# Kernel tuning notes

Measured on AMD Instinct MI355X. Metric: run time of the kernel, lower is better.

## Reference

```python
import jax, jax.numpy as jnp
import numpy as np


def _ste_round(x):
    # straight-through rounding (Brevitas-style QAT)
    return x + jax.lax.stop_gradient(jnp.round(x) - x)


def _q_act_signed(x, s):
    # 4-bit signed activation fake-quant: int range [-8, 7]
    return jnp.clip(_ste_round(x / s), -8, 7) * s


def _q_relu(x, s):
    # QuantReLU: relu then 4-bit unsigned fake-quant, int range [0, 15]
    return jnp.clip(_ste_round(jax.nn.relu(x) / s), 0, 15) * s


def _q_weight(w):
    # 4-bit narrow-range per-tensor weight quant: scale = max|w|/7, range [-7, 7]
    s = jnp.max(jnp.abs(w)) / 7.0
    return jnp.clip(_ste_round(w / s), -7, 7) * s, s


def _q_bias(b, s):
    # Int32Bias: bias quantized at scale = act_scale * weight_scale (int32 range, no clamp)
    return _ste_round(b / s) * s


def _conv(x, w):
    return jax.lax.conv_general_dilated(
        x, w, (1, 1), 'VALID', dimension_numbers=('NCHW', 'OIHW', 'NCHW'))


def _maxpool_ceil(x, k=3, st=2):
    # MaxPool2d(3, 2, ceil_mode=True): pad right/bottom with -inf as needed
    def pad(n):
        out = -(-(n - k) // st) + 1
        return max(0, (out - 1) * st + k - n)
    ph, pw = pad(x.shape[2]), pad(x.shape[3])
    return jax.lax.reduce_window(
        x, -jnp.inf, jax.lax.max, (1, 1, k, k), (1, 1, st, st),
        [(0, 0), (0, 0), (0, ph), (0, pw)])


def reference(x, w1, b1, w2, b2, w3, b3, fw1, fb1, bw, bb, cw, cb,
              s_inp, s1, s2, s3, s4, s_bbox, s_conf):
    a = s_inp[0]
    x = _q_act_signed(x, a)                               # quant_inp
    # conv1 + relu1 + pool1
    wq, ws = _q_weight(w1)
    x = _conv(x, wq) + _q_bias(b1, a * ws)[None, :, None, None]
    a = s1[0]
    x = _maxpool_ceil(_q_relu(x, a))                      # [B,28,11,11]
    # conv2 + relu2 + pool2
    wq, ws = _q_weight(w2)
    x = _conv(x, wq) + _q_bias(b2, a * ws)[None, :, None, None]
    a = s2[0]
    x = _maxpool_ceil(_q_relu(x, a))                      # [B,48,4,4]
    # conv3 + relu3
    wq, ws = _q_weight(w3)
    x = _conv(x, wq) + _q_bias(b3, a * ws)[None, :, None, None]
    a = s3[0]
    x = _q_relu(x, a)                                     # [B,64,3,3]
    # QuantFlatten: transpose(3,2) then flatten -> [B, 576]
    x = jnp.transpose(x, (0, 1, 3, 2)).reshape(x.shape[0], -1)
    # fc1 + relu4
    wq, ws = _q_weight(fw1)
    x = x @ wq.T + _q_bias(fb1, a * ws)
    a = s4[0]
    x = _q_relu(x, a)                                     # [B,128]
    # heads
    wq, ws = _q_weight(bw)
    bbox = x @ wq.T + _q_bias(bb, a * ws)                 # [B,4]
    wq, ws = _q_weight(cw)
    conf = x @ wq.T + _q_bias(cb, a * ws)                 # [B,2]
    bbox = _q_act_signed(bbox, s_bbox[0])
    conf = _q_act_signed(conf, s_conf[0])
    return bbox, conf


def setup_inputs() -> dict:
    key = jax.random.key(0)
    ks = jax.random.split(key, 14)
    B = 4096
    f32 = jnp.float32
    return {
        'x': jax.random.normal(ks[0], (B, 3, 24, 24), f32),
        'w1': jax.random.normal(ks[1], (28, 3, 3, 3), f32) * 0.1,
        'b1': jax.random.normal(ks[2], (28,), f32) * 0.1,
        'w2': jax.random.normal(ks[3], (48, 28, 3, 3), f32) * 0.1,
        'b2': jax.random.normal(ks[4], (48,), f32) * 0.1,
        'w3': jax.random.normal(ks[5], (64, 48, 2, 2), f32) * 0.1,
        'b3': jax.random.normal(ks[6], (64,), f32) * 0.1,
        'fw1': jax.random.normal(ks[7], (128, 576), f32) * 0.05,
        'fb1': jax.random.normal(ks[8], (128,), f32) * 0.1,
        'bw': jax.random.normal(ks[9], (4, 128), f32) * 0.1,
        'bb': jax.random.normal(ks[10], (4,), f32) * 0.1,
        'cw': jax.random.normal(ks[11], (2, 128), f32) * 0.1,
        'cb': jax.random.normal(ks[12], (2,), f32) * 0.1,
        's_inp': jnp.ones((1,), f32),
        's1': jnp.ones((1,), f32),
        's2': jnp.ones((1,), f32),
        's3': jnp.ones((1,), f32),
        's4': jnp.ones((1,), f32),
        's_bbox': jnp.ones((1,), f32),
        's_conf': jnp.ones((1,), f32),
    }
```

## Files before the change

### kernel.cpp

```cpp
#include <hip/hip_runtime.h>
#include <hip/hip_bf16.h>
#include <math.h>

typedef __attribute__((ext_vector_type(8))) short bf16x8v;
typedef __attribute__((ext_vector_type(4))) float f32x4v;

__device__ __forceinline__ float loadT(const void* p, size_t i, int isbf) {
    if (isbf) return __bfloat162float(((const __hip_bfloat16*)p)[i]);
    return ((const float*)p)[i];
}
__device__ __forceinline__ float quantw(float v, float s) {
    return fminf(fmaxf(rintf(v / s), -7.f), 7.f) * s;
}
__device__ __forceinline__ float quantwc(float v, float s) {
    return fminf(fmaxf(rintf(v / s), -7.f), 7.f);
}
__device__ __forceinline__ float qbias(float v, float den) {
    return rintf(v / den) * den;
}
__device__ __forceinline__ float qrelu(float v, float s) {
    return fminf(fmaxf(rintf(fmaxf(v, 0.f) / s), 0.f), 15.f) * s;
}
__device__ __forceinline__ float qcode(float Cint, float bcode, float p, float snext) {
    float v = (Cint + bcode) * p;
    return fminf(fmaxf(rintf(fmaxf(v, 0.f) / snext), 0.f), 15.f);
}
__device__ __forceinline__ float bfbits(unsigned u) {
    return __uint_as_float(u << 16);
}

__global__ void k_beacon(float* out, float code) {
    if (threadIdx.x == 0 && blockIdx.x == 0) out[0] = code;
}

static constexpr int W1C  = 16;
static constexpr int B1C  = 772;
static constexpr int B2C  = 800;
static constexpr int B3C  = 848;
static constexpr int FB1C = 912;
static constexpr int BBC  = 1040;
static constexpr int CBC  = 1044;
static constexpr int FW1B = 1048;
static constexpr int W2B  = 37912;
static constexpr int W3B  = 44056;
static constexpr int BWC  = 50200;
static constexpr int CWC  = 50712;
static constexpr int PMAXF = 51000;

__device__ __constant__ int d_CHK[6]  = { 1, 4, 4, 24, 1, 1 };
__device__ __constant__ int d_POFF[7] = { 0, 1, 5, 9, 33, 34, 35 };

__global__ __launch_bounds__(256) void k_scale(
    const void* w1, const void* w2, const void* w3, const void* fw1,
    const void* bw, const void* cw,
    const void* s0p, const void* s1p, const void* s2p, const void* s3p,
    const void* s4p, const void* s5p, const void* s6p,
    float* __restrict__ ws)
{
    __shared__ float red[256];
    __shared__ float shisbf;
    const int tid = threadIdx.x, blk = blockIdx.x;
    if (tid < 64) {
        const unsigned short* hb = (const unsigned short*)w1;
        const float a = fabsf(bfbits((unsigned)hb[2 * tid]));
        const unsigned long long bz = __ballot(a == 0.f);
        const unsigned long long bs = __ballot(a > 1e-8f && a < 1e4f);
        if (tid == 0) {
            const int zeros = __popcll(bz), sane = __popcll(bs);
            shisbf = (zeros < 40 && sane >= 40) ? 1.f : 0.f;
        }
    }
    __syncthreads();
    const int isbf = shisbf > 0.5f;
    if (blk == 0) {
        if (tid == 7) ws[15] = shisbf;
        if (tid < 7) {
            const void* sp[7] = { s0p, s1p, s2p, s3p, s4p, s5p, s6p };
            const void* p = sp[tid];
            float v = *(const float*)p;
            float a = fabsf(v);
            if (!(a > 1e-6f && a < 1e6f)) {
                double d = *(const double*)p;
                double ad = fabs(d);
                if (ad > 1e-6 && ad < 1e6) v = (float)d;
                else v = bfbits((unsigned)(*(const unsigned short*)p));
            }
            ws[tid] = v;
        }
    }
    int j = 0;
    while (j < 5 && blk >= d_POFF[j + 1]) ++j;
    const int c = blk - d_POFF[j];
    const void* wp[6] = { w1, w2, w3, fw1, bw, cw };
    const int   wn[6] = { 756, 12096, 12288, 73728, 512, 256 };
    const int nw = wn[j];
    const int len = (nw + d_CHK[j] - 1) / d_CHK[j];
    const int i0 = c * len, i1 = min(i0 + len, nw);
    float m = 0.f;
    for (int i = i0 + tid; i < i1; i += 256)
        m = fmaxf(m, fabsf(loadT(wp[j], i, isbf)));
    red[tid] = m; __syncthreads();
    for (int o = 128; o > 0; o >>= 1) {
        if (tid < o) red[tid] = fmaxf(red[tid], red[tid + o]);
        __syncthreads();
    }
    if (tid == 0) ws[PMAXF + blk] = red[0];
}

__global__ __launch_bounds__(256) void k_quant(
    const void* w1, const void* b1, const void* w2, const void* b2,
    const void* w3, const void* b3, const void* fw1, const void* fb1,
    const void* bw, const void* bb, const void* cw, const void* cb,
    float* __restrict__ ws)
{
    const int tid = threadIdx.x, blk = blockIdx.x;
    const int isbf = ws[15] > 0.5f;
    auto getscale = [&](int j) {
        float m = 0.f;
        for (int t = d_POFF[j]; t < d_POFF[j + 1]; ++t)
            m = fmaxf(m, ws[PMAXF + t]);
        return m / 7.0f;
    };

    if (blk < 24) {
        const float s = getscale(3);
        const int i0 = blk * 3072, i1 = min(i0 + 3072, 73728);
        __hip_bfloat16* dst = (__hip_bfloat16*)(ws + FW1B);
        for (int i = i0 + tid; i < i1; i += 256) {
            const float q = quantwc(loadT(fw1, i, isbf), s);
            const int o = i / 576, f = i % 576;
            const int c = f / 9, fw_ = (f % 9) / 3, fh = f % 3;
            const int kk = c * 9 + fh * 3 + fw_;
            dst[(kk >> 1) * 256 + o * 2 + (kk & 1)] = __float2bfloat16(q);
        }
    } else if (blk < 28) {
        const float s = getscale(1);
        const int c = blk - 24;
        const int i0 = c * 3024, i1 = min(i0 + 3024, 12096);
        __hip_bfloat16* dst = (__hip_bfloat16*)(ws + W2B);
        for (int i = i0 + tid; i < i1; i += 256) {
            const float q = quantwc(loadT(w2, i, isbf), s);
            const int n = i / 252, k = i % 252;
            dst[n * 256 + k] = __float2bfloat16(q);
        }
        if (c == 0) {
            for (int i = tid; i < 192; i += 256) {
                const int n = i / 4, k = 252 + (i % 4);
                dst[n * 256 + k] = __float2bfloat16(0.f);
            }
        }
    } else if (blk < 32) {
        const float s = getscale(2);
        const int c = blk - 28;
        const int i0 = c * 3072, i1 = min(i0 + 3072, 12288);
        __hip_bfloat16* dst = (__hip_bfloat16*)(ws + W3B);
        for (int i = i0 + tid; i < i1; i += 256)
            dst[i] = __float2bfloat16(quantwc(loadT(w3, i, isbf), s));
    } else if (blk == 32) {
        const float s = getscale(0);
        for (int i = tid; i < 756; i += 256)
            ws[W1C + i] = quantwc(loadT(w1, i, isbf), s);
    } else {
        const float s0 = getscale(0), s1 = getscale(1), s2 = getscale(2);
        const float s3 = getscale(3), s4 = getscale(4), s5 = getscale(5);
        const float sa0 = ws[0], sa1 = ws[1], sa2 = ws[2], sa3 = ws[3], sa4 = ws[4];
        for (int i = tid; i < 512; i += 256) ws[BWC + i] = quantwc(loadT(bw, i, isbf), s4);
        for (int i = tid; i < 256; i += 256) ws[CWC + i] = quantwc(loadT(cw, i, isbf), s5);
        if (tid < 28)  ws[B1C + tid]  = rintf(loadT(b1, tid, isbf)  / (sa0 * s0));
        if (tid < 48)  ws[B2C + tid]  = rintf(loadT(b2, tid, isbf)  / (sa1 * s1));
        if (tid < 64)  ws[B3C + tid]  = rintf(loadT(b3, tid, isbf)  / (sa2 * s2));
        if (tid < 128) ws[FB1C + tid] = rintf(loadT(fb1, tid, isbf) / (sa3 * s3));
        if (tid < 4)   ws[BBC + tid]  = rintf(loadT(bb, tid, isbf)  / (sa4 * s4));
        if (tid < 2)   ws[CBC + tid]  = rintf(loadT(cb, tid, isbf)  / (sa4 * s5));
        if (tid == 0) {
            ws[8]  = sa0 * s0;
            ws[9]  = sa1 * s1;
            ws[10] = sa2 * s2;
            ws[11] = sa3 * s3;
            ws[12] = sa4 * s4;
            ws[13] = sa4 * s5;
        }
    }
}

__global__ __launch_bounds__(256, 4) void k_net(
    const void* __restrict__ x, const float* __restrict__ wsr,
    float* __restrict__ outp)
{
    __shared__ __align__(16) float U[9952];
    const int tid = threadIdx.x, b = blockIdx.x;
    const float sa0 = wsr[0], sa1 = wsr[1], sa2 = wsr[2], sa3 = wsr[3];
    const float sa4 = wsr[4], sab = wsr[5], sac = wsr[6];
    const float p1 = wsr[8], p2 = wsr[9], p3 = wsr[10], p4 = wsr[11];
    const float pB = wsr[12], pC = wsr[13];
    const int isbf = wsr[15] > 0.5f;
    constexpr int ACT2F = 0, ACT3F = 768, ACT1F = 1344;
    constexpr int XQF = 3040, W1F = 4840, B1F = 5596;
    constexpr int AF = 3040, BFP = 4960, C2IF = 5920, B2CF = 9889;
    constexpr int W3F = 3040, B3CF = 9184;
    constexpr int PF = 3040, A4F = 3296, PARTF = 3424;

    for (int i = tid; i < 1728; i += 256) {
        const float v = loadT(x, (size_t)b * 1728 + i, isbf);
        const int ci = i / 576, r = (i % 576) / 24, c = i % 24;
        U[XQF + ci * 600 + r * 25 + c] = fminf(fmaxf(rintf(v / sa0), -8.f), 7.f);
    }
    for (int i = tid; i < 756; i += 256) U[W1F + i] = wsr[W1C + i];
    if (tid < 28) U[B1F + tid] = wsr[B1C + tid];
    __syncthreads();

    {
        __hip_bfloat16* act1w = (__hip_bfloat16*)(U + ACT1F);
        for (int item = tid; item < 308; item += 256) {
            const int o = item / 11, ph = item % 11;
            const int r0 = 2 * ph;
            const bool row2ok = (r0 + 2) < 22;
            float wk[27];
            #pragma unroll
            for (int i = 0; i < 27; ++i) wk[i] = U[W1F + o * 27 + i];
            const float bc = U[B1F + o];
            float w5[45];
            #pragma unroll
            for (int ci = 0; ci < 3; ++ci)
                #pragma unroll
                for (int ir = 0; ir < 5; ++ir)
                    #pragma unroll
                    for (int j = 0; j < 2; ++j)
                        w5[ci * 15 + ir * 3 + j] =
                            (r0 + ir < 24) ? U[XQF + ci * 600 + (r0 + ir) * 25 + j] : 0.f;
            float accP = -1e30f, accC = -1e30f;
            for (int c = 0; c < 22; ++c) {
                #pragma unroll
                for (int ci = 0; ci < 3; ++ci)
                    #pragma unroll
                    for (int ir = 0; ir < 5; ++ir)
                        w5[ci * 15 + ir * 3 + 2] =
                            (r0 + ir < 24) ? U[XQF + ci * 600 + (r0 + ir) * 25 + (c + 2)] : 0.f;
                float a0 = 0.f, a1 = 0.f, a2 = 0.f;
                #pragma unroll
                for (int ci = 0; ci < 3; ++ci)
                    #pragma unroll
                    for (int kr = 0; kr < 3; ++kr)
                        #pragma unroll
                        for (int kc = 0; kc < 3; ++kc) {
                            const float w = wk[ci * 9 + kr * 3 + kc];
                            a0 = fmaf(w5[ci * 15 + (kr + 0) * 3 + kc], w, a0);
                            a1 = fmaf(w5[ci * 15 + (kr + 1) * 3 + kc], w, a1);
                            a2 = fmaf(w5[ci * 15 + (kr + 2) * 3 + kc], w, a2);
                        }
                float cm = fmaxf(a0, a1);
                cm = row2ok ? fmaxf(cm, a2) : cm;
                if ((c & 1) == 0) {
                    if (c >= 2)
                        act1w[o * 121 + ph * 11 + (c / 2 - 1)] =
                            __float2bfloat16(qcode(fmaxf(accP, cm), bc, p1, sa1));
                    accC = cm;
                } else {
                    accC = fmaxf(accC, cm);
                    accP = accC;
                }
                #pragma unroll
                for (int ci = 0; ci < 3; ++ci)
                    #pragma unroll
                    for (int ir = 0; ir < 5; ++ir) {
                        w5[ci * 15 + ir * 3 + 0] = w5[ci * 15 + ir * 3 + 1];
                        w5[ci * 15 + ir * 3 + 1] = w5[ci * 15 + ir * 3 + 2];
                    }
            }
            act1w[o * 121 + ph * 11 + 10] =
                __float2bfloat16(qcode(accP, bc, p1, sa1));
        }
    }
    __syncthreads();

    {
        const unsigned short* act1u = (const unsigned short*)(U + ACT1F);
        unsigned short* Au = (unsigned short*)(U + AF);
        unsigned short* Bu = (unsigned short*)(U + BFP);
        const unsigned short* w2u = (const unsigned short*)(wsr + W2B);
        if (tid < 48) U[B2CF + tid] = wsr[B2C + tid];
        const int kloc = tid & 31, g = tid >> 5;
        const int wv = tid >> 6, lane = tid & 63;
        f32x4v acc[5];
        #pragma unroll
        for (int j = 0; j < 5; ++j) { acc[j][0]=0.f; acc[j][1]=0.f; acc[j][2]=0.f; acc[j][3]=0.f; }
        for (int kk = 0; kk < 8; ++kk) {
            const int k = kk * 32 + kloc;
            const bool kok = (k < 252);
            const int ci = kok ? k / 9 : 0;
            const int kr = kok ? (k % 9) / 3 : 0, kc = kok ? k % 3 : 0;
            #pragma unroll
            for (int e = 0; e < 12; ++e) {
                const int s = g + 8 * e;
                unsigned short v = 0;
                if (kok && s < 81) {
                    const int r = s / 9, c = s % 9;
                    v = act1u[ci * 121 + (r + kr) * 11 + (c + kc)];
                }
                Au[s * 40 + kloc] = v;
            }
            #pragma unroll
            for (int e = 0; e < 6; ++e) {
                const int n = g + 8 * e;
                Bu[n * 40 + kloc] = w2u[n * 256 + k];
            }
            __syncthreads();
            #pragma unroll
            for (int j = 0; j < 5; ++j) {
                const int t = wv + 4 * j;
                if (t < 18) {
                    const int tm = t / 3, tn = t % 3;
                    bf16x8v af = *(const bf16x8v*)(Au + (tm * 16 + (lane & 15)) * 40 + (lane >> 4) * 8);
                    bf16x8v bfv = *(const bf16x8v*)(Bu + (tn * 16 + (lane & 15)) * 40 + (lane >> 4) * 8);
                    acc[j] = __builtin_amdgcn_mfma_f32_16x16x32_bf16(af, bfv, acc[j], 0, 0, 0);
                }
            }
            __syncthreads();
        }
        #pragma unroll
        for (int j = 0; j < 5; ++j) {
            const int t = wv + 4 * j;
            if (t < 18) {
                const int tm = t / 3, tn = t % 3;
                const int col = tn * 16 + (lane & 15);
                #pragma unroll
                for (int r = 0; r < 4; ++r) {
                    const int row = tm * 16 + (lane >> 4) * 4 + r;
                    if (row < 81) U[C2IF + row * 49 + col] = acc[j][r];
                }
            }
        }
        __syncthreads();
        for (int id = tid; id < 768; id += 256) {
            const int ch = id >> 4, pp = id & 15, ph = pp >> 2, pw = pp & 3;
            float mx = -1e30f;
            #pragma unroll
            for (int r = 0; r < 3; ++r)
                #pragma unroll
                for (int c = 0; c < 3; ++c)
                    mx = fmaxf(mx, U[C2IF + ((2 * ph + r) * 9 + (2 * pw + c)) * 49 + ch]);
            U[ACT2F + ch * 16 + pp] = qcode(mx, U[B2CF + ch], p2, sa2);
        }
    }
    __syncthreads();

    for (int i = tid; i < 6144; i += 256) U[W3F + i] = wsr[W3B + i];
    if (tid < 64) U[B3CF + tid] = wsr[B3C + tid];
    __syncthreads();
    if (tid < 192) {
        const int o = tid / 3, hq = tid % 3;
        const unsigned* w3u = (const unsigned*)(U + W3F);
        float a0 = 0.f, a1 = 0.f, a2 = 0.f;
        for (int ci = 0; ci < 48; ++ci) {
            const unsigned pa = w3u[o * 96 + ci * 2];
            const unsigned pb = w3u[o * 96 + ci * 2 + 1];
            const float w00 = bfbits(pa & 0xffffu), w01 = bfbits(pa >> 16);
            const float w10 = bfbits(pb & 0xffffu), w11 = bfbits(pb >> 16);
            const int xb = ACT2F + ci * 16;
            const f32x4v r0 = *(const f32x4v*)(U + xb + hq * 4);
            const f32x4v r1 = *(const f32x4v*)(U + xb + (hq + 1) * 4);
            a0 = fmaf(r0[0], w00, a0); a0 = fmaf(r0[1], w01, a0);
            a0 = fmaf(r1[0], w10, a0); a0 = fmaf(r1[1], w11, a0);
            a1 = fmaf(r0[1], w00, a1); a1 = fmaf(r0[2], w01, a1);
            a1 = fmaf(r1[1], w10, a1); a1 = fmaf(r1[2], w11, a1);
            a2 = fmaf(r0[2], w00, a2); a2 = fmaf(r0[3], w01, a2);
            a2 = fmaf(r1[2], w10, a2); a2 = fmaf(r1[3], w11, a2);
        }
        const float bc = U[B3CF + o];
        U[ACT3F + o * 9 + hq * 3 + 0] = qcode(a0, bc, p3, sa3);
        U[ACT3F + o * 9 + hq * 3 + 1] = qcode(a1, bc, p3, sa3);
        U[ACT3F + o * 9 + hq * 3 + 2] = qcode(a2, bc, p3, sa3);
    }
    __syncthreads();

    {
        const int o = tid & 127, half = tid >> 7;
        const unsigned* fwp = (const unsigned*)(wsr + FW1B);
        float acc = 0.f;
        const int kp0 = half * 144;
        for (int kp = kp0; kp < kp0 + 144; ++kp) {
            const unsigned pr = fwp[kp * 128 + o];
            acc = fmaf(U[ACT3F + 2 * kp],     bfbits(pr & 0xffffu), acc);
            acc = fmaf(U[ACT3F + 2 * kp + 1], bfbits(pr >> 16),     acc);
        }
        U[PF + tid] = acc;
    }
    __syncthreads();
    if (tid < 128) {
        const float C = U[PF + tid] + U[PF + 128 + tid];
        U[A4F + tid] = qcode(C, wsr[FB1C + tid], p4, sa4);
    }
    __syncthreads();

    if (tid < 96) {
        const int d = tid >> 4, gq = tid & 15;
        const float* hw = (d < 4) ? (wsr + BWC + d * 128) : (wsr + CWC + (d - 4) * 128);
        float p = 0.f;
        #pragma unroll
        for (int k = 0; k < 8; ++k)
            p = fmaf(U[A4F + gq * 8 + k], hw[gq * 8 + k], p);
        U[PARTF + d * 16 + gq] = p;
    }
    __syncthreads();
    if (tid < 6) {
        float C = (tid < 4) ? wsr[BBC + tid] : wsr[CBC + (tid - 4)];
        for (int g = 0; g < 16; ++g) C += U[PARTF + tid * 16 + g];
        if (tid < 4) {
            const float val = C * pB;
            outp[(size_t)b * 4 + tid] = fminf(fmaxf(rintf(val / sab), -8.f), 7.f) * sab;
        } else {
            const float val = C * pC;
            outp[16384 + (size_t)b * 2 + (tid - 4)] =
                fminf(fmaxf(rintf(val / sac), -8.f), 7.f) * sac;
        }
    }
}

__global__ __launch_bounds__(256) void k_net_fb(
    const void* __restrict__ x,
    const void* __restrict__ w1,  const void* __restrict__ b1,
    const void* __restrict__ w2,  const void* __restrict__ b2,
    const void* __restrict__ w3,  const void* __restrict__ b3,
    const void* __restrict__ fw1, const void* __restrict__ fb1,
    const void* __restrict__ bw,  const void* __restrict__ bb,
    const void* __restrict__ cw,  const void* __restrict__ cb,
    const void* __restrict__ s0p, const void* __restrict__ s1p,
    const void* __restrict__ s2p, const void* __restrict__ s3p,
    const void* __restrict__ s4p, const void* __restrict__ s5p,
    const void* __restrict__ s6p,
    float* __restrict__ outp)
{
    __shared__ float U[16000];
    __shared__ float swsh[8];
    __shared__ float sash[8];
    const int tid = threadIdx.x;
    const int b   = blockIdx.x;
    constexpr int RED = 0, XQ = 0, W1Q = 1728, B1Q = 2484, C1 = 2512;
    constexpr int ACT1 = 9288, WB = 0, C2 = 12676, ACT2 = 14620, ACT3 = 15388;
    constexpr int A4 = 0, PART = 128;

    if (tid == 0) {
        const unsigned short* hb = (const unsigned short*)w1;
        int zeros = 0, sane = 0;
        for (int i = 0; i < 64; ++i) {
            unsigned short u = hb[2 * i];
            float v = __uint_as_float(((unsigned int)u) << 16);
            float a = fabsf(v);
            if (a == 0.f) zeros++;
            else if (a > 1e-8f && a < 1e4f) sane++;
        }
        swsh[7] = (zeros < 40 && sane >= 40) ? 1.f : 0.f;
        const void* sp[7] = { s0p, s1p, s2p, s3p, s4p, s5p, s6p };
        for (int j = 0; j < 7; ++j) {
            float v = *(const float*)sp[j];
            float a = fabsf(v);
            if (!(a > 1e-6f && a < 1e6f)) {
                double d = *(const double*)sp[j];
                double ad = fabs(d);
                if (ad > 1e-6 && ad < 1e6) v = (float)d;
                else {
                    unsigned short u = *(const unsigned short*)sp[j];
                    v = __uint_as_float(((unsigned int)u) << 16);
                }
            }
            sash[j] = v;
        }
    }
    __syncthreads();
    const int isbf = swsh[7] > 0.5f;
    {
        const void* wp[6] = { w1, w2, w3, fw1, bw, cw };
        const int   wn[6] = { 756, 12096, 12288, 73728, 512, 256 };
        for (int j = 0; j < 6; ++j) {
            float m = 0.f;
            for (int i = tid; i < wn[j]; i += 256)
                m = fmaxf(m, fabsf(loadT(wp[j], i, isbf)));
            U[RED + tid] = m; __syncthreads();
            for (int o = 128; o > 0; o >>= 1) {
                if (tid < o) U[RED + tid] = fmaxf(U[RED + tid], U[RED + tid + o]);
                __syncthreads();
            }
            if (tid == 0) swsh[j] = U[RED] / 7.0f;
            __syncthreads();
        }
    }
    const float sa0 = sash[0], sa1 = sash[1], sa2 = sash[2], sa3 = sash[3];
    const float sa4 = sash[4], sab = sash[5], sac = sash[6];
    const float sw1s = swsh[0], sw2s = swsh[1], sw3s = swsh[2];
    const float sw4s = swsh[3], swbs = swsh[4], swcs = swsh[5];

    for (int i = tid; i < 1728; i += 256) {
        float v = loadT(x, (size_t)b * 1728 + i, isbf);
        U[XQ + i] = fminf(fmaxf(rintf(v / sa0), -8.f), 7.f) * sa0;
    }
    for (int i = tid; i < 756; i += 256) U[W1Q + i] = quantw(loadT(w1, i, isbf), sw1s);
    {
        const float den = sa0 * sw1s;
        for (int i = tid; i < 28; i += 256) U[B1Q + i] = qbias(loadT(b1, i, isbf), den);
    }
    __syncthreads();

    for (int g = 0; g < 2; ++g) {
        const int obase = g * 14;
        for (int idx = tid; idx < 308; idx += 256) {
            const int ol = idx / 22, r = idx % 22, o = obase + ol;
            for (int c = 0; c < 22; ++c) {
                float acc = 0.f;
                #pragma unroll
                for (int ci = 0; ci < 3; ++ci)
                    #pragma unroll
                    for (int kr = 0; kr < 3; ++kr)
                        #pragma unroll
                        for (int kc = 0; kc < 3; ++kc)
                            acc = fmaf(U[XQ + ci * 576 + (r + kr) * 24 + (c + kc)],
                                       U[W1Q + o * 27 + ci * 9 + kr * 3 + kc], acc);
                U[C1 + ol * 484 + r * 22 + c] = acc + U[B1Q + o];
            }
        }
        __syncthreads();
        for (int i = tid; i < 1694; i += 256) {
            const int ol = i / 121, rem = i % 121, ph = rem / 11, pw = rem % 11;
            const int r0 = 2 * ph, c0 = 2 * pw;
            const int r1 = min(r0 + 3, 22), c1 = min(c0 + 3, 22);
            float mx = -1e30f;
            for (int r = r0; r < r1; ++r)
                for (int c = c0; c < c1; ++c)
                    mx = fmaxf(mx, U[C1 + ol * 484 + r * 22 + c]);
            U[ACT1 + (obase + ol) * 121 + rem] = qrelu(mx, sa1);
        }
        __syncthreads();
    }

    for (int h = 0; h < 2; ++h) {
        const int obase = h * 24;
        for (int i = tid; i < 6048; i += 256)
            U[WB + i] = quantw(loadT(w2, (size_t)h * 6048 + i, isbf), sw2s);
        {
            const float den = sa1 * sw2s;
            for (int i = tid; i < 24; i += 256)
                U[WB + 6048 + i] = qbias(loadT(b2, obase + i, isbf), den);
        }
        __syncthreads();
        for (int idx = tid; idx < 216; idx += 256) {
            const int ol = idx / 9, r = idx % 9;
            for (int c = 0; c < 9; ++c) {
                float acc = 0.f;
                for (int ci = 0; ci < 28; ++ci)
                    #pragma unroll
                    for (int kr = 0; kr < 3; ++kr)
                        #pragma unroll
                        for (int kc = 0; kc < 3; ++kc)
                            acc = fmaf(U[ACT1 + ci * 121 + (r + kr) * 11 + (c + kc)],
                                       U[WB + ol * 252 + ci * 9 + kr * 3 + kc], acc);
                U[C2 + ol * 81 + r * 9 + c] = acc + U[WB + 6048 + ol];
            }
        }
        __syncthreads();
        for (int i = tid; i < 384; i += 256) {
            const int ol = i / 16, ph = (i % 16) / 4, pw = i % 4;
            float mx = -1e30f;
            #pragma unroll
            for (int r = 0; r < 3; ++r)
                #pragma unroll
                for (int c = 0; c < 3; ++c)
                    mx = fmaxf(mx, U[C2 + ol * 81 + (2 * ph + r) * 9 + (2 * pw + c)]);
            U[ACT2 + (obase + ol) * 16 + (i % 16)] = qrelu(mx, sa2);
        }
        __syncthreads();
    }

    for (int h = 0; h < 2; ++h) {
        const int obase = h * 32;
        for (int i = tid; i < 6144; i += 256)
            U[WB + i] = quantw(loadT(w3, (size_t)h * 6144 + i, isbf), sw3s);
        {
            const float den = sa2 * sw3s;
            for (int i = tid; i < 32; i += 256)
                U[WB + 6144 + i] = qbias(loadT(b3, obase + i, isbf), den);
        }
        __syncthreads();
        for (int idx = tid; idx < 288; idx += 256) {
            const int ol = idx / 9, hh = (idx % 9) / 3, ww = idx % 3;
            float acc = 0.f;
            for (int ci = 0; ci < 48; ++ci) {
                const int xb2 = ACT2 + ci * 16;
                const int wb2 = WB + ol * 192 + ci * 4;
                acc = fmaf(U[xb2 + hh * 4 + ww],           U[wb2 + 0], acc);
                acc = fmaf(U[xb2 + hh * 4 + ww + 1],       U[wb2 + 1], acc);
                acc = fmaf(U[xb2 + (hh + 1) * 4 + ww],     U[wb2 + 2], acc);
                acc = fmaf(U[xb2 + (hh + 1) * 4 + ww + 1], U[wb2 + 3], acc);
            }
            acc += U[WB + 6144 + ol];
            U[ACT3 + (obase + ol) * 9 + hh * 3 + ww] = qrelu(acc, sa3);
        }
        __syncthreads();
    }

    {
        const int wave = tid >> 6, lane = tid & 63;
        const float den = sa3 * sw4s;
        for (int oo = 0; oo < 32; ++oo) {
            const int o = wave * 32 + oo;
            float acc = 0.f;
            #pragma unroll
            for (int j = 0; j < 9; ++j) {
                const int f = lane + 64 * j;
                const int c = f / 9, fw = (f % 9) / 3, fh = f % 3;
                const float av = U[ACT3 + c * 9 + fh * 3 + fw];
                const float wv = quantw(loadT(fw1, (size_t)o * 576 + f, isbf), sw4s);
                acc = fmaf(av, wv, acc);
            }
            #pragma unroll
            for (int off = 32; off > 0; off >>= 1)
                acc += __shfl_down(acc, off);
            if (lane == 0) {
                acc += qbias(loadT(fb1, o, isbf), den);
                U[A4 + o] = qrelu(acc, sa4);
            }
        }
    }
    __syncthreads();

    if (tid < 96) {
        const int d = tid >> 4, g = tid & 15;
        const void* hw = (d < 4) ? bw : cw;
        const int row = (d < 4) ? d : d - 4;
        const float swh = (d < 4) ? swbs : swcs;
        float p = 0.f;
        #pragma unroll
        for (int k = 0; k < 8; ++k) {
            const int kk = g * 8 + k;
            p = fmaf(U[A4 + kk], quantw(loadT(hw, row * 128 + kk, isbf), swh), p);
        }
        U[PART + d * 16 + g] = p;
    }
    __syncthreads();
    if (tid < 6) {
        const int d = tid;
        float acc;
        if (d < 4) acc = qbias(loadT(bb, d, isbf), sa4 * swbs);
        else       acc = qbias(loadT(cb, d - 4, isbf), sa4 * swcs);
        for (int g = 0; g < 16; ++g) acc += U[PART + d * 16 + g];
        if (d < 4) outp[(size_t)b * 4 + d] = fminf(fmaxf(rintf(acc / sab), -8.f), 7.f) * sab;
        else outp[16384 + (size_t)b * 2 + (d - 4)] = fminf(fmaxf(rintf(acc / sac), -8.f), 7.f) * sac;
    }
}

extern "C" void kernel_launch(void* const* d_in, const int* in_sizes, int n_in,
                              void* d_out, int out_size, void* d_ws, size_t ws_size,
                              hipStream_t stream)
{
    float* out = (float*)d_out;
    const int expect[20] = { 7077888, 756, 28, 12096, 48, 12288, 64, 73728, 128,
                             512, 4, 256, 2, 1, 1, 1, 1, 1, 1, 1 };
    if (n_in < 20) { k_beacon<<<1, 64, 0, stream>>>(out, 9000.f); return; }
    for (int i = 0; i < 20; ++i)
        if (in_sizes[i] != expect[i]) {
            k_beacon<<<1, 64, 0, stream>>>(out, 2000.f + 10.f * i);
            return;
        }

    if (ws_size >= (size_t)100000 * sizeof(float)) {
        float* ws = (float*)d_ws;
        k_scale<<<35, 256, 0, stream>>>(
            d_in[1], d_in[3], d_in[5], d_in[7], d_in[9], d_in[11],
            d_in[13], d_in[14], d_in[15], d_in[16], d_in[17], d_in[18], d_in[19],
            ws);
        k_quant<<<34, 256, 0, stream>>>(
            d_in[1], d_in[2], d_in[3], d_in[4], d_in[5], d_in[6],
            d_in[7], d_in[8], d_in[9], d_in[10], d_in[11], d_in[12],
            ws);
        k_net<<<4096, 256, 0, stream>>>(d_in[0], ws, out);
    } else {
        k_net_fb<<<4096, 256, 0, stream>>>(
            d_in[0], d_in[1], d_in[2], d_in[3], d_in[4], d_in[5], d_in[6],
            d_in[7], d_in[8], d_in[9], d_in[10], d_in[11], d_in[12],
            d_in[13], d_in[14], d_in[15], d_in[16], d_in[17], d_in[18], d_in[19],
            out);
    }
}
```

Measured before the change: 205.0 us.

## Split conv1 pooling into row-wise conv pass plus separate vertical max pass

Conv1 now runs as 616 work items, one per output channel and conv row, instead of 308 items each computing three rows per pooled row. Each item keeps a 3x3 register window, applies the horizontal pool max and writes fp16 intermediates to shared memory. A second pass does the vertical max, bias and quantization into the bf16 activation buffer. The aim is to spread the work across all 256 threads instead of leaving a second, mostly idle iteration, and to remove the redundant overlapping row computation. The cost is an extra barrier, an fp16 intermediate round trip through LDS with possible rounding of pre-bias sums, and more shared memory. The conv3 weight copy is also vectorized to 16-byte loads.

Measured after the change: 200.5 us, median of 2. -2.2%, faster.

```diff
diff --git a/kernel.cpp b/kernel.cpp
--- a/kernel.cpp
+++ b/kernel.cpp
@@ -195,7 +195,7 @@
     const float pB = wsr[12], pC = wsr[13];
     const int isbf = wsr[15] > 0.5f;
     constexpr int ACT2F = 0, ACT3F = 768, ACT1F = 1344;
-    constexpr int XQF = 3040, W1F = 4840, B1F = 5596;
+    constexpr int XQF = 3040, W1F = 4840, B1F = 5596, CMF = 5632;
     constexpr int AF = 3040, BFP = 4960, C2IF = 5920, B2CF = 9889;
     constexpr int W3F = 3040, B3CF = 9184;
     constexpr int PF = 3040, A4F = 3296, PARTF = 3424;
@@ -210,65 +210,60 @@
     __syncthreads();
 
     {
-        __hip_bfloat16* act1w = (__hip_bfloat16*)(U + ACT1F);
-        for (int item = tid; item < 308; item += 256) {
-            const int o = item / 11, ph = item % 11;
-            const int r0 = 2 * ph;
-            const bool row2ok = (r0 + 2) < 22;
+        _Float16* cm16 = (_Float16*)(U + CMF);
+        #pragma unroll 1
+        for (int item = tid; item < 616; item += 256) {
+            const int o = item / 22, r = item % 22;
             float wk[27];
             #pragma unroll
             for (int i = 0; i < 27; ++i) wk[i] = U[W1F + o * 27 + i];
-            const float bc = U[B1F + o];
-            float w5[45];
+            float w9[27];
             #pragma unroll
             for (int ci = 0; ci < 3; ++ci)
                 #pragma unroll
-                for (int ir = 0; ir < 5; ++ir)
+                for (int kr = 0; kr < 3; ++kr)
                     #pragma unroll
                     for (int j = 0; j < 2; ++j)
-                        w5[ci * 15 + ir * 3 + j] =
-                            (r0 + ir < 24) ? U[XQF + ci * 600 + (r0 + ir) * 25 + j] : 0.f;
-            float accP = -1e30f, accC = -1e30f;
+                        w9[ci * 9 + kr * 3 + j] = U[XQF + ci * 600 + (r + kr) * 25 + j];
+            float accP = 0.f, accC = 0.f;
+            _Float16* dst = cm16 + o * 242 + r * 11;
+            #pragma unroll
             for (int c = 0; c < 22; ++c) {
+                const int snew = (c + 2) % 3;
                 #pragma unroll
                 for (int ci = 0; ci < 3; ++ci)
                     #pragma unroll
-                    for (int ir = 0; ir < 5; ++ir)
-                        w5[ci * 15 + ir * 3 + 2] =
-                            (r0 + ir < 24) ? U[XQF + ci * 600 + (r0 + ir) * 25 + (c + 2)] : 0.f;
-                float a0 = 0.f, a1 = 0.f, a2 = 0.f;
+                    for (int kr = 0; kr < 3; ++kr)
+                        w9[ci * 9 + kr * 3 + snew] =
+                            U[XQF + ci * 600 + (r + kr) * 25 + (c + 2)];
+                float cm = 0.f;
                 #pragma unroll
                 for (int ci = 0; ci < 3; ++ci)
                     #pragma unroll
                     for (int kr = 0; kr < 3; ++kr)
                         #pragma unroll
-                        for (int kc = 0; kc < 3; ++kc) {
-                            const float w = wk[ci * 9 + kr * 3 + kc];
-                            a0 = fmaf(w5[ci * 15 + (kr + 0) * 3 + kc], w, a0);
-                            a1 = fmaf(w5[ci * 15 + (kr + 1) * 3 + kc], w, a1);
-                            a2 = fmaf(w5[ci * 15 + (kr + 2) * 3 + kc], w, a2);
-                        }
-                float cm = fmaxf(a0, a1);
-                cm = row2ok ? fmaxf(cm, a2) : cm;
-                if ((c & 1) == 0) {
-                    if (c >= 2)
-                        act1w[o * 121 + ph * 11 + (c / 2 - 1)] =
-                            __float2bfloat16(qcode(fmaxf(accP, cm), bc, p1, sa1));
-                    accC = cm;
-                } else {
-                    accC = fmaxf(accC, cm);
-                    accP = accC;
-                }
-                #pragma unroll
-                for (int ci = 0; ci < 3; ++ci)
-                    #pragma unroll
-                    for (int ir = 0; ir < 5; ++ir) {
-                        w5[ci * 15 + ir * 3 + 0] = w5[ci * 15 + ir * 3 + 1];
-                        w5[ci * 15 + ir * 3 + 1] = w5[ci * 15 + ir * 3 + 2];
-                    }
-            }
-            act1w[o * 121 + ph * 11 + 10] =
-                __float2bfloat16(qcode(accP, bc, p1, sa1));
+                        for (int kc = 0; kc < 3; ++kc)
+                            cm = fmaf(w9[ci * 9 + kr * 3 + ((c + kc) % 3)],
+                                      wk[ci * 9 + kr * 3 + kc], cm);
+                if (c == 0) accC = cm;
+                else if (c & 1) { accC = fmaxf(accC, cm); accP = accC; }
+                else { dst[c / 2 - 1] = (_Float16)fmaxf(accP, cm); accC = cm; }
+            }
+            dst[10] = (_Float16)accP;
+        }
+    }
+    __syncthreads();
+    {
+        const _Float16* cm16 = (const _Float16*)(U + CMF);
+        __hip_bfloat16* act1w = (__hip_bfloat16*)(U + ACT1F);
+        for (int id = tid; id < 3388; id += 256) {
+            const int o = id / 121, rem = id % 121, ph = rem / 11, pw = rem % 11;
+            const int rr0 = 2 * ph;
+            const _Float16* src = cm16 + o * 242 + pw;
+            float mx = fmaxf((float)src[rr0 * 11], (float)src[(rr0 + 1) * 11]);
+            if (rr0 + 2 < 22) mx = fmaxf(mx, (float)src[(rr0 + 2) * 11]);
+            act1w[o * 121 + ph * 11 + pw] =
+                __float2bfloat16(qcode(mx, U[B1F + o], p1, sa1));
         }
     }
     __syncthreads();
@@ -344,7 +339,11 @@
     }
     __syncthreads();
 
-    for (int i = tid; i < 6144; i += 256) U[W3F + i] = wsr[W3B + i];
+    {
+        const f32x4v* src = (const f32x4v*)(wsr + W3B);
+        f32x4v* dstv = (f32x4v*)(U + W3F);
+        for (int i = tid; i < 1536; i += 256) dstv[i] = src[i];
+    }
     if (tid < 64) U[B3CF + tid] = wsr[B3C + tid];
     __syncthreads();
     if (tid < 192) {
```
